# Performance work log

Measured on AMD Instinct MI355X. Metric: run time of the kernel, lower is better.

The kernel has to match this reference:

```python
import jax, jax.numpy as jnp
import numpy as np

EPS = 1e-06
S = 0.025
ALPHA = 0.98
DELTA = 2.0
R = 0.5


def setup_inputs() -> dict:
    key = jax.random.key(0)
    # mel spectrogram magnitudes: non-negative
    x = jax.random.uniform(key, (32, 8192, 128), dtype=jnp.float32)
    return {"x": x}


def reference(x):
    # EMA smoother over time: M[0] = x[0]; M[t] = (1-s)*M[t-1] + s*x[t]
    # x: [B, T, F] -> scan over time with carry [B, F]
    def step(m_prev, x_t):
        m = (1.0 - S) * m_prev + S * x_t
        return m, m

    x_t_major = jnp.moveaxis(x[:, 1:, :], 1, 0)  # [T-1, B, F]
    _, ms = jax.lax.scan(step, x[:, 0, :], x_t_major)  # ms: [T-1, B, F]
    M = jnp.concatenate([x[:, :1, :], jnp.moveaxis(ms, 0, 1)], axis=1)  # [B, T, F]

    # PCEN: (x / (M + eps)^alpha + delta)^r - delta^r
    out = (x / jnp.power(M + EPS, ALPHA) + DELTA) ** R - DELTA ** R
    return out
```

## Files before the change

### kernel.cpp

```cpp
#include <hip/hip_runtime.h>
#include <math.h>


#define BB 32
#define TT 8192
#define FF 128
#define CC 32
#define KC (TT / CC)
#define AA 0.975f
#define SS 0.025f

using f32x2 = __attribute__((ext_vector_type(2))) float;

constexpr float pow_a32() {
    float p = 1.0f;
    for (int i = 0; i < 32; ++i) p *= 0.975f;
    return p;
}
constexpr float P32 = pow_a32();

__device__ __forceinline__ float pcen_out(float xv, float m) {
    float p = __builtin_amdgcn_exp2f(-0.98f * __builtin_amdgcn_logf(m + 1e-6f));
    return sqrtf(fmaf(xv, p, 2.0f)) - 1.41421356237309505f;
}

__global__ __launch_bounds__(256) void pcen_k1(const float* __restrict__ x,
                                               float* __restrict__ q) {
    const int tid = threadIdx.x;
    const int row = blockIdx.x * 4 + (tid >> 6);
    const int b   = row >> 8;
    const int k   = row & (KC - 1);
    const int f2  = tid & 63;

    const f32x2* xp = (const f32x2*)(x + ((size_t)b * TT + (size_t)k * CC) * FF) + f2;
    f32x2 v[CC];
    #pragma unroll
    for (int j = 0; j < CC; ++j) v[j] = xp[(size_t)j * (FF / 2)];

    float m0, m1;
    if (k == 0) { m0 = v[0][0];      m1 = v[0][1]; }
    else        { m0 = SS * v[0][0]; m1 = SS * v[0][1]; }
    #pragma unroll
    for (int j = 1; j < CC; ++j) {
        m0 = fmaf(AA, m0, SS * v[j][0]);
        m1 = fmaf(AA, m1, SS * v[j][1]);
    }

    f32x2* qp = (f32x2*)(q + ((size_t)b * KC + k) * FF) + f2;
    f32x2 o; o[0] = m0; o[1] = m1;
    *qp = o;
}

__global__ __launch_bounds__(256) void pcen_k2(float* __restrict__ q) {
    const int c = blockIdx.x * 256 + threadIdx.x;
    const int b = c >> 7;
    const int f = c & (FF - 1);
    float* qp = q + (size_t)b * KC * FF + f;

    float carry = 0.0f;
    for (int k0 = 0; k0 < KC; k0 += 8) {
        float t[8];
        #pragma unroll
        for (int u = 0; u < 8; ++u) t[u] = qp[(size_t)(k0 + u) * FF];
        #pragma unroll
        for (int u = 0; u < 8; ++u) {
            const int k = k0 + u;
            if (k == 0) {
                qp[0] = 0.0f;
                carry = t[0];
            } else {
                qp[(size_t)k * FF] = carry;
                carry = fmaf(P32, carry, t[u]);
            }
        }
    }
}

__global__ __launch_bounds__(256) void pcen_k3(const float* __restrict__ x,
                                               const float* __restrict__ q,
                                               float* __restrict__ out) {
    const int tid = threadIdx.x;
    const int row = blockIdx.x * 4 + (tid >> 6);
    const int b   = row >> 8;
    const int k   = row & (KC - 1);
    const int f2  = tid & 63;

    const size_t base = ((size_t)b * TT + (size_t)k * CC) * FF;
    const f32x2* xp = (const f32x2*)(x + base) + f2;
    f32x2*       op = (f32x2*)(out + base) + f2;

    f32x2 v[CC];
    #pragma unroll
    for (int j = 0; j < CC; ++j) v[j] = xp[(size_t)j * (FF / 2)];

    float m0, m1;
    if (k == 0) {
        m0 = v[0][0]; m1 = v[0][1];
    } else {
        const f32x2 mn = *((const f32x2*)(q + ((size_t)b * KC + k) * FF) + f2);
        m0 = fmaf(AA, mn[0], SS * v[0][0]);
        m1 = fmaf(AA, mn[1], SS * v[0][1]);
    }
    {
        f32x2 o; o[0] = pcen_out(v[0][0], m0); o[1] = pcen_out(v[0][1], m1);
        __builtin_nontemporal_store(o, op);
    }
    #pragma unroll
    for (int j = 1; j < CC; ++j) {
        m0 = fmaf(AA, m0, SS * v[j][0]);
        m1 = fmaf(AA, m1, SS * v[j][1]);
        f32x2 o; o[0] = pcen_out(v[j][0], m0); o[1] = pcen_out(v[j][1], m1);
        __builtin_nontemporal_store(o, op + (size_t)j * (FF / 2));
    }
}

__global__ __launch_bounds__(128) void pcen_fallback(const float* __restrict__ x,
                                                     float* __restrict__ out) {
    const int job = blockIdx.x;
    const int b   = job >> 5;
    const int k   = job & 31;
    const int f   = threadIdx.x;
    const int t0  = k * 256;
    const size_t base = ((size_t)b * TT + t0) * FF + f;
    const float* xp = x + base;
    float*       op = out + base;
    float m;
    if (k == 0) {
        float xv = xp[0];
        m = xv;
        op[0] = pcen_out(xv, m);
    } else {
        const float* wp = xp - (size_t)256 * FF;
        m = wp[0];
        #pragma unroll 8
        for (int j = 1; j < 256; ++j) m = fmaf(AA, m, SS * wp[(size_t)j * FF]);
        float xv = xp[0];
        m = fmaf(AA, m, SS * xv);
        op[0] = pcen_out(xv, m);
    }
    #pragma unroll 4
    for (int j = 1; j < 256; ++j) {
        float xv = xp[(size_t)j * FF];
        m = fmaf(AA, m, SS * xv);
        op[(size_t)j * FF] = pcen_out(xv, m);
    }
}

extern "C" void kernel_launch(void* const* d_in, const int* in_sizes, int n_in,
                              void* d_out, int out_size, void* d_ws, size_t ws_size,
                              hipStream_t stream) {
    const float* x = (const float*)d_in[0];
    float* out = (float*)d_out;
    (void)in_sizes; (void)n_in; (void)out_size;

    const size_t q_bytes = (size_t)BB * KC * FF * sizeof(float);
    if (ws_size >= q_bytes) {
        float* q = (float*)d_ws;
        pcen_k1<<<(BB * KC) / 4, 256, 0, stream>>>(x, q);
        pcen_k2<<<(BB * FF) / 256, 256, 0, stream>>>(q);
        pcen_k3<<<(BB * KC) / 4, 256, 0, stream>>>(x, q, out);
    } else {
        pcen_fallback<<<BB * 32, 128, 0, stream>>>(x, out);
    }
}
```

Measured before the change: 74.05 us.

## Parallelize chunk-carry scan across wavefront lanes and software-pipeline chunk loads

The middle kernel's serial 256-step carry scan per (batch, feature) column becomes a wavefront-wide parallel scan. Each of 64 lanes composes 4 chunk summaries, then a log-step shuffle scan with squared decay factors combines them, and each lane writes back its exclusive prefixes. The first and third kernels now load x in blocks of 8 rows and prefetch the next block while computing the current one, instead of holding all 32 rows in registers. This cuts the serial latency of the small kernel and register pressure in the big ones, but launches 64x more threads for the scan and issues strided uncoalesced reads.

```diff
diff --git a/kernel.cpp b/kernel.cpp
--- a/kernel.cpp
+++ b/kernel.cpp
@@ -12,12 +12,13 @@
 
 using f32x2 = __attribute__((ext_vector_type(2))) float;
 
-constexpr float pow_a32() {
+constexpr float powf_n(float a, int n) {
     float p = 1.0f;
-    for (int i = 0; i < 32; ++i) p *= 0.975f;
+    for (int i = 0; i < n; ++i) p *= a;
     return p;
 }
-constexpr float P32 = pow_a32();
+constexpr float P32  = powf_n(0.975f, 32);
+constexpr float P128 = powf_n(0.975f, 128);
 
 __device__ __forceinline__ float pcen_out(float xv, float m) {
     float p = __builtin_amdgcn_exp2f(-0.98f * __builtin_amdgcn_logf(m + 1e-6f));
@@ -33,47 +34,66 @@
     const int f2  = tid & 63;
 
     const f32x2* xp = (const f32x2*)(x + ((size_t)b * TT + (size_t)k * CC) * FF) + f2;
-    f32x2 v[CC];
+
+    f32x2 v[8];
     #pragma unroll
-    for (int j = 0; j < CC; ++j) v[j] = xp[(size_t)j * (FF / 2)];
+    for (int u = 0; u < 8; ++u) v[u] = xp[(size_t)u * (FF / 2)];
 
-    float m0, m1;
-    if (k == 0) { m0 = v[0][0];      m1 = v[0][1]; }
-    else        { m0 = SS * v[0][0]; m1 = SS * v[0][1]; }
+    float m0 = (k == 0) ? v[0][0] : SS * v[0][0];
+    float m1 = (k == 0) ? v[0][1] : SS * v[0][1];
+
     #pragma unroll
-    for (int j = 1; j < CC; ++j) {
-        m0 = fmaf(AA, m0, SS * v[j][0]);
-        m1 = fmaf(AA, m1, SS * v[j][1]);
+    for (int jb = 0; jb < CC; jb += 8) {
+        f32x2 w[8];
+        #pragma unroll
+        for (int u = 0; u < 8; ++u) w[u] = v[u];
+        if (jb + 8 < CC) {
+            #pragma unroll
+            for (int u = 0; u < 8; ++u) v[u] = xp[(size_t)(jb + 8 + u) * (FF / 2)];
+        }
+        #pragma unroll
+        for (int u = 0; u < 8; ++u) {
+            if (jb == 0 && u == 0) continue;
+            m0 = fmaf(AA, m0, SS * w[u][0]);
+            m1 = fmaf(AA, m1, SS * w[u][1]);
+        }
     }
 
-    f32x2* qp = (f32x2*)(q + ((size_t)b * KC + k) * FF) + f2;
     f32x2 o; o[0] = m0; o[1] = m1;
-    *qp = o;
+    *((f32x2*)(q + ((size_t)b * KC + k) * FF) + f2) = o;
 }
 
 __global__ __launch_bounds__(256) void pcen_k2(float* __restrict__ q) {
-    const int c = blockIdx.x * 256 + threadIdx.x;
-    const int b = c >> 7;
-    const int f = c & (FF - 1);
+    const int gid  = blockIdx.x * 256 + threadIdx.x;
+    const int wid  = gid >> 6;
+    const int lane = threadIdx.x & 63;
+    const int b    = wid >> 7;
+    const int f    = wid & (FF - 1);
     float* qp = q + (size_t)b * KC * FF + f;
 
-    float carry = 0.0f;
-    for (int k0 = 0; k0 < KC; k0 += 8) {
-        float t[8];
-        #pragma unroll
-        for (int u = 0; u < 8; ++u) t[u] = qp[(size_t)(k0 + u) * FF];
-        #pragma unroll
-        for (int u = 0; u < 8; ++u) {
-            const int k = k0 + u;
-            if (k == 0) {
-                qp[0] = 0.0f;
-                carry = t[0];
-            } else {
-                qp[(size_t)k * FF] = carry;
-                carry = fmaf(P32, carry, t[u]);
-            }
-        }
+    const int k0 = 4 * lane;
+    float t0 = qp[(size_t)(k0 + 0) * FF];
+    float t1 = qp[(size_t)(k0 + 1) * FF];
+    float t2 = qp[(size_t)(k0 + 2) * FF];
+    float t3 = qp[(size_t)(k0 + 3) * FF];
+
+    float v = fmaf(fmaf(fmaf(t0, P32, t1), P32, t2), P32, t3);
+
+    float fac = P128;
+    #pragma unroll
+    for (int d = 1; d < 64; d <<= 1) {
+        float up = __shfl_up(v, d, 64);
+        if (lane >= d) v = fmaf(fac, up, v);
+        fac *= fac;
     }
+
+    float I = __shfl_up(v, 1, 64);
+    if (lane == 0) I = 0.0f;
+
+    qp[(size_t)(k0 + 0) * FF] = I; I = fmaf(P32, I, t0);
+    qp[(size_t)(k0 + 1) * FF] = I; I = fmaf(P32, I, t1);
+    qp[(size_t)(k0 + 2) * FF] = I; I = fmaf(P32, I, t2);
+    qp[(size_t)(k0 + 3) * FF] = I;
 }
 
 __global__ __launch_bounds__(256) void pcen_k3(const float* __restrict__ x,
@@ -89,9 +109,9 @@
     const f32x2* xp = (const f32x2*)(x + base) + f2;
     f32x2*       op = (f32x2*)(out + base) + f2;
 
-    f32x2 v[CC];
+    f32x2 v[8];
     #pragma unroll
-    for (int j = 0; j < CC; ++j) v[j] = xp[(size_t)j * (FF / 2)];
+    for (int u = 0; u < 8; ++u) v[u] = xp[(size_t)u * (FF / 2)];
 
     float m0, m1;
     if (k == 0) {
@@ -101,16 +121,27 @@
         m0 = fmaf(AA, mn[0], SS * v[0][0]);
         m1 = fmaf(AA, mn[1], SS * v[0][1]);
     }
-    {
-        f32x2 o; o[0] = pcen_out(v[0][0], m0); o[1] = pcen_out(v[0][1], m1);
-        __builtin_nontemporal_store(o, op);
-    }
+
     #pragma unroll
-    for (int j = 1; j < CC; ++j) {
-        m0 = fmaf(AA, m0, SS * v[j][0]);
-        m1 = fmaf(AA, m1, SS * v[j][1]);
-        f32x2 o; o[0] = pcen_out(v[j][0], m0); o[1] = pcen_out(v[j][1], m1);
-        __builtin_nontemporal_store(o, op + (size_t)j * (FF / 2));
+    for (int jb = 0; jb < CC; jb += 8) {
+        f32x2 w[8];
+        #pragma unroll
+        for (int u = 0; u < 8; ++u) w[u] = v[u];
+        if (jb + 8 < CC) {
+            #pragma unroll
+            for (int u = 0; u < 8; ++u) v[u] = xp[(size_t)(jb + 8 + u) * (FF / 2)];
+        }
+        #pragma unroll
+        for (int u = 0; u < 8; ++u) {
+            if (!(jb == 0 && u == 0)) {
+                m0 = fmaf(AA, m0, SS * w[u][0]);
+                m1 = fmaf(AA, m1, SS * w[u][1]);
+            }
+            f32x2 o;
+            o[0] = pcen_out(w[u][0], m0);
+            o[1] = pcen_out(w[u][1], m1);
+            __builtin_nontemporal_store(o, op + (size_t)(jb + u) * (FF / 2));
+        }
     }
 }
 
@@ -157,7 +188,7 @@
     if (ws_size >= q_bytes) {
         float* q = (float*)d_ws;
         pcen_k1<<<(BB * KC) / 4, 256, 0, stream>>>(x, q);
-        pcen_k2<<<(BB * FF) / 256, 256, 0, stream>>>(q);
+        pcen_k2<<<(BB * FF * 64) / 256, 256, 0, stream>>>(q);
         pcen_k3<<<(BB * KC) / 4, 256, 0, stream>>>(x, q, out);
     } else {
         pcen_fallback<<<BB * 32, 128, 0, stream>>>(x, out);
```

New measurement: 81.66 us. 10.3% more time.

## Replace serial carry-scan kernel with truncated windowed carry reconstruction

Applied to the files above, without the earlier changes.

Removes the separate carry-propagation kernel, which ran a serial scan over chunk summaries on very few blocks. Chunks are now 64 steps, split into four 16-step sub-chunks that are combined through LDS. The incoming EMA state for each chunk is rebuilt in the output kernel as a weighted sum of the previous six chunk summaries, using decay powers of 0.975. History older than 384 steps is dropped. The intent is to eliminate a latency-bound launch, at the cost of a small truncation error (weight about 0.975^384) and a few extra summary reads per block.

```diff
diff --git a/kernel.cpp b/kernel.cpp
--- a/kernel.cpp
+++ b/kernel.cpp
@@ -5,19 +5,26 @@
 #define BB 32
 #define TT 8192
 #define FF 128
-#define CC 32
+#define CC 64
 #define KC (TT / CC)
+#define SUB 16
+#define NH  (CC / SUB)
+#define WW 6
 #define AA 0.975f
 #define SS 0.025f
 
 using f32x2 = __attribute__((ext_vector_type(2))) float;
 
-constexpr float pow_a32() {
+constexpr float powf_n(float a, int n) {
     float p = 1.0f;
-    for (int i = 0; i < 32; ++i) p *= 0.975f;
+    for (int i = 0; i < n; ++i) p *= a;
     return p;
 }
-constexpr float P32 = pow_a32();
+constexpr float P16 = powf_n(0.975f, 16);
+constexpr float WQ[WW] = {
+    powf_n(0.975f, 0),   powf_n(0.975f, 64),  powf_n(0.975f, 128),
+    powf_n(0.975f, 192), powf_n(0.975f, 256), powf_n(0.975f, 320)
+};
 
 __device__ __forceinline__ float pcen_out(float xv, float m) {
     float p = __builtin_amdgcn_exp2f(-0.98f * __builtin_amdgcn_logf(m + 1e-6f));
@@ -26,91 +33,112 @@
 
 __global__ __launch_bounds__(256) void pcen_k1(const float* __restrict__ x,
                                                float* __restrict__ q) {
+    __shared__ f32x2 lds[NH][64];
     const int tid = threadIdx.x;
-    const int row = blockIdx.x * 4 + (tid >> 6);
-    const int b   = row >> 8;
-    const int k   = row & (KC - 1);
+    const int h   = tid >> 6;
     const int f2  = tid & 63;
+    const int bid = blockIdx.x;
+    const int b   = bid >> 7;
+    const int k   = bid & (KC - 1);
 
-    const f32x2* xp = (const f32x2*)(x + ((size_t)b * TT + (size_t)k * CC) * FF) + f2;
-    f32x2 v[CC];
+    const f32x2* xp = (const f32x2*)(x + ((size_t)b * TT + (size_t)k * CC
+                                          + (size_t)h * SUB) * FF) + f2;
+    f32x2 v[SUB];
     #pragma unroll
-    for (int j = 0; j < CC; ++j) v[j] = xp[(size_t)j * (FF / 2)];
+    for (int i = 0; i < SUB; ++i) v[i] = xp[(size_t)i * (FF / 2)];
 
-    float m0, m1;
-    if (k == 0) { m0 = v[0][0];      m1 = v[0][1]; }
-    else        { m0 = SS * v[0][0]; m1 = SS * v[0][1]; }
+    float s0, s1;
+    if (k == 0 && h == 0) { s0 = v[0][0];      s1 = v[0][1]; }
+    else                  { s0 = SS * v[0][0]; s1 = SS * v[0][1]; }
     #pragma unroll
-    for (int j = 1; j < CC; ++j) {
-        m0 = fmaf(AA, m0, SS * v[j][0]);
-        m1 = fmaf(AA, m1, SS * v[j][1]);
+    for (int i = 1; i < SUB; ++i) {
+        s0 = fmaf(AA, s0, SS * v[i][0]);
+        s1 = fmaf(AA, s1, SS * v[i][1]);
     }
 
-    f32x2* qp = (f32x2*)(q + ((size_t)b * KC + k) * FF) + f2;
-    f32x2 o; o[0] = m0; o[1] = m1;
-    *qp = o;
-}
+    f32x2 sv; sv[0] = s0; sv[1] = s1;
+    lds[h][f2] = sv;
+    __syncthreads();
 
-__global__ __launch_bounds__(256) void pcen_k2(float* __restrict__ q) {
-    const int c = blockIdx.x * 256 + threadIdx.x;
-    const int b = c >> 7;
-    const int f = c & (FF - 1);
-    float* qp = q + (size_t)b * KC * FF + f;
-
-    float carry = 0.0f;
-    for (int k0 = 0; k0 < KC; k0 += 8) {
-        float t[8];
-        #pragma unroll
-        for (int u = 0; u < 8; ++u) t[u] = qp[(size_t)(k0 + u) * FF];
-        #pragma unroll
-        for (int u = 0; u < 8; ++u) {
-            const int k = k0 + u;
-            if (k == 0) {
-                qp[0] = 0.0f;
-                carry = t[0];
-            } else {
-                qp[(size_t)k * FF] = carry;
-                carry = fmaf(P32, carry, t[u]);
-            }
-        }
+    if (h == 0) {
+        f32x2 a0 = lds[0][f2], a1 = lds[1][f2], a2 = lds[2][f2], a3 = lds[3][f2];
+        f32x2 o;
+        o[0] = fmaf(fmaf(fmaf(a0[0], P16, a1[0]), P16, a2[0]), P16, a3[0]);
+        o[1] = fmaf(fmaf(fmaf(a0[1], P16, a1[1]), P16, a2[1]), P16, a3[1]);
+        *((f32x2*)(q + ((size_t)b * KC + k) * FF) + f2) = o;
     }
 }
 
 __global__ __launch_bounds__(256) void pcen_k3(const float* __restrict__ x,
                                                const float* __restrict__ q,
                                                float* __restrict__ out) {
+    __shared__ f32x2 lds[NH][64];
     const int tid = threadIdx.x;
-    const int row = blockIdx.x * 4 + (tid >> 6);
-    const int b   = row >> 8;
-    const int k   = row & (KC - 1);
+    const int h   = tid >> 6;
     const int f2  = tid & 63;
+    const int bid = blockIdx.x;
+    const int b   = bid >> 7;
+    const int k   = bid & (KC - 1);
 
-    const size_t base = ((size_t)b * TT + (size_t)k * CC) * FF;
-    const f32x2* xp = (const f32x2*)(x + base) + f2;
-    f32x2*       op = (f32x2*)(out + base) + f2;
+    const size_t tbase = (size_t)b * TT + (size_t)k * CC + (size_t)h * SUB;
+    const f32x2* xp = (const f32x2*)(x + tbase * FF) + f2;
+    f32x2*       op = (f32x2*)(out + tbase * FF) + f2;
 
-    f32x2 v[CC];
+    f32x2 v[SUB];
     #pragma unroll
-    for (int j = 0; j < CC; ++j) v[j] = xp[(size_t)j * (FF / 2)];
+    for (int i = 0; i < SUB; ++i) v[i] = xp[(size_t)i * (FF / 2)];
 
-    float m0, m1;
-    if (k == 0) {
-        m0 = v[0][0]; m1 = v[0][1];
-    } else {
-        const f32x2 mn = *((const f32x2*)(q + ((size_t)b * KC + k) * FF) + f2);
-        m0 = fmaf(AA, mn[0], SS * v[0][0]);
-        m1 = fmaf(AA, mn[1], SS * v[0][1]);
+    float c0 = 0.0f, c1 = 0.0f;
+    {
+        const f32x2* qp = (const f32x2*)(q + (size_t)b * KC * FF) + f2;
+        #pragma unroll
+        for (int jj = 1; jj <= WW; ++jj) {
+            if (jj <= k) {
+                f32x2 qv = qp[(size_t)(k - jj) * (FF / 2)];
+                c0 = fmaf(WQ[jj - 1], qv[0], c0);
+                c1 = fmaf(WQ[jj - 1], qv[1], c1);
+            }
+        }
     }
+
+    float s0, s1;
+    if (k == 0 && h == 0) { s0 = v[0][0];      s1 = v[0][1]; }
+    else                  { s0 = SS * v[0][0]; s1 = SS * v[0][1]; }
+    #pragma unroll
+    for (int i = 1; i < SUB; ++i) {
+        s0 = fmaf(AA, s0, SS * v[i][0]);
+        s1 = fmaf(AA, s1, SS * v[i][1]);
+    }
+    f32x2 sv; sv[0] = s0; sv[1] = s1;
+    lds[h][f2] = sv;
+    __syncthreads();
+
+    float m0 = c0, m1 = c1;
+    for (int g = 0; g < h; ++g) {
+        f32x2 sg = lds[g][f2];
+        m0 = fmaf(P16, m0, sg[0]);
+        m1 = fmaf(P16, m1, sg[1]);
+    }
+
     {
-        f32x2 o; o[0] = pcen_out(v[0][0], m0); o[1] = pcen_out(v[0][1], m1);
+        f32x2 o;
+        if (k == 0 && h == 0) { m0 = v[0][0]; m1 = v[0][1]; }
+        else {
+            m0 = fmaf(AA, m0, SS * v[0][0]);
+            m1 = fmaf(AA, m1, SS * v[0][1]);
+        }
+        o[0] = pcen_out(v[0][0], m0);
+        o[1] = pcen_out(v[0][1], m1);
         __builtin_nontemporal_store(o, op);
     }
     #pragma unroll
-    for (int j = 1; j < CC; ++j) {
-        m0 = fmaf(AA, m0, SS * v[j][0]);
-        m1 = fmaf(AA, m1, SS * v[j][1]);
-        f32x2 o; o[0] = pcen_out(v[j][0], m0); o[1] = pcen_out(v[j][1], m1);
-        __builtin_nontemporal_store(o, op + (size_t)j * (FF / 2));
+    for (int i = 1; i < SUB; ++i) {
+        m0 = fmaf(AA, m0, SS * v[i][0]);
+        m1 = fmaf(AA, m1, SS * v[i][1]);
+        f32x2 o;
+        o[0] = pcen_out(v[i][0], m0);
+        o[1] = pcen_out(v[i][1], m1);
+        __builtin_nontemporal_store(o, op + (size_t)i * (FF / 2));
     }
 }
 
@@ -156,9 +184,8 @@
     const size_t q_bytes = (size_t)BB * KC * FF * sizeof(float);
     if (ws_size >= q_bytes) {
         float* q = (float*)d_ws;
-        pcen_k1<<<(BB * KC) / 4, 256, 0, stream>>>(x, q);
-        pcen_k2<<<(BB * FF) / 256, 256, 0, stream>>>(q);
-        pcen_k3<<<(BB * KC) / 4, 256, 0, stream>>>(x, q, out);
+        pcen_k1<<<BB * KC, 256, 0, stream>>>(x, q);
+        pcen_k3<<<BB * KC, 256, 0, stream>>>(x, q, out);
     } else {
         pcen_fallback<<<BB * 32, 128, 0, stream>>>(x, out);
     }
```

Result: faster. 68.36 us (-7.7%).
